# Performance work log

Hardware: AMD Instinct MI355X
Metric: run time of the kernel (lower is better)

Reference implementation:

```python
import jax, jax.numpy as jnp
import numpy as np

B = 32      # graphs per batch
N_NODES = 1024  # nodes per graph
K = 16      # top-k edges per node


def setup_inputs() -> dict:
    key = jax.random.key(0)
    k1, k2 = jax.random.split(key)
    x = jax.random.normal(k1, (B * N_NODES, 128), dtype=jnp.float32) * 0.1
    W = jax.random.normal(k2, (128, 64), dtype=jnp.float32) * (1.0 / np.sqrt(128))
    b = jnp.zeros((64,), dtype=jnp.float32)
    temperature = jnp.asarray(4.0, dtype=jnp.float32)
    return {"x": x, "W": W, "b": b, "temperature": temperature}


def reference(x, W, b, temperature):
    # Encoder: linear node embedding. out: [B*n, C]
    out = x @ W + b
    C = out.shape[-1]
    # Per-graph features, detached as in the original (graph_x = out[...].detach())
    h = jax.lax.stop_gradient(out).reshape(B, N_NODES, C)
    # Pairwise squared euclidean distances per graph: d[b,i,j] = ||h_i - h_j||^2
    sq = jnp.sum(h * h, axis=-1)  # [B, n]
    d_e = sq[:, :, None] + sq[:, None, :] - 2.0 * jnp.einsum('bic,bjc->bij', h, h)
    logits = jnp.exp(-temperature * d_e)  # [B, n, n]
    # Gumbel-noised top-k edge sampling
    z = jax.random.gumbel(jax.random.key(1), logits.shape, logits.dtype)
    _, edges_hat = jax.lax.top_k(logits + z, K)  # [B, n, K] int32
    # Build global edge index with cumulative per-graph node offsets
    offsets = (jnp.arange(B, dtype=jnp.int32) * N_NODES)[:, None, None]  # [B,1,1]
    rows = jnp.broadcast_to(jnp.arange(N_NODES, dtype=jnp.int32)[None, :, None] + offsets,
                            (B, N_NODES, K))
    cols = edges_hat.astype(jnp.int32) + offsets
    edges_idx = jnp.stack((rows.reshape(-1), cols.reshape(-1)))  # [2, B*n*K]
    return out, edges_idx
```

## Files before the change

### kernel.cpp

```cpp
#include <hip/hip_runtime.h>
#include <math.h>

#define OUT_ELEMS 2097152
#define EDGE_ELEMS 524288

__device__ __forceinline__ unsigned int rotl32(unsigned int x, int r){
  return (x << r) | (x >> (32 - r));
}

__device__ __forceinline__ unsigned int tf_bits_part(unsigned int e){
  unsigned int x0 = 0u, x1 = e;
  const unsigned int ks1 = 1u;
  const unsigned int ks2 = 0x1BD11BDBu;
  x1 += ks1;
#define TFR(r) { x0 += x1; x1 = rotl32(x1, r); x1 ^= x0; }
  TFR(13) TFR(15) TFR(26) TFR(6)
  x0 += ks1; x1 += ks2 + 1u;
  TFR(17) TFR(29) TFR(16) TFR(24)
  x0 += ks2; x1 += 0u + 2u;
  TFR(13) TFR(15) TFR(26) TFR(6)
  x0 += 0u;  x1 += ks1 + 3u;
  TFR(17) TFR(29) TFR(16) TFR(24)
  x0 += ks1; x1 += ks2 + 4u;
  TFR(13) TFR(15) TFR(26) TFR(6)
  x0 += ks2; x1 += 0u + 5u;
#undef TFR
  return x0 ^ x1;
}

__device__ __forceinline__ double rcp64(double x){
  double r;
  asm("v_rcp_f64 %0, %1" : "=v"(r) : "v"(x));
  double e = fma(-x, r, 1.0); r = fma(r, e, r);
  e = fma(-x, r, 1.0); r = fma(r, e, r);
  return r;
}

__device__ __forceinline__ double fast_exp(double x){
  double fn = __builtin_rint(x * 1.4426950408889634);
  int n = (int)fn;
  double r = fma(fn, -0.6931471803691238, x);
  r = fma(fn, -1.9082149292705877e-10, r);
  double p = 2.7557319223985893e-06;
  p = fma(r, p, 2.4801587301587302e-05);
  p = fma(r, p, 1.9841269841269841e-04);
  p = fma(r, p, 1.3888888888888889e-03);
  p = fma(r, p, 8.3333333333333333e-03);
  p = fma(r, p, 4.1666666666666664e-02);
  p = fma(r, p, 1.6666666666666666e-01);
  p = fma(r, p, 0.5);
  p = fma(r, p, 1.0);
  p = fma(r, p, 1.0);
  double scale = __longlong_as_double(((long long)(n + 1023)) << 52);
  return p * scale;
}

__device__ __forceinline__ double fast_log(double x){
  long long bx = __double_as_longlong(x);
  long long e = (bx >> 52) - 1023;
  double m = __longlong_as_double((bx & 0xFFFFFFFFFFFFFll) |
                                  0x3FF0000000000000ll);
  int big = m > 1.4142135623730951;
  m = big ? 0.5 * m : m;
  e += big;
  double s = (m - 1.0) * rcp64(m + 1.0);
  double s2 = s * s;
  double p = fma(s2, 2.0/11.0, 2.0/9.0);
  p = fma(s2, p, 2.0/7.0);
  p = fma(s2, p, 2.0/5.0);
  p = fma(s2, p, 2.0/3.0);
  double lm = fma(s * s2, p, 2.0 * s);
  return fma((double)e, 0.6931471805599453, lm);
}

__device__ __forceinline__ unsigned long long score_cand32(
    const float* __restrict__ og, const float* __restrict__ hrowf,
    unsigned int jc, unsigned int base, double Td, bool act){
  const float4* cp4 = (const float4*)(og + ((size_t)jc << 6));
  const float4* hp4 = (const float4*)hrowf;
  float a0 = 0.0f, a1 = 0.0f, a2 = 0.0f, a3 = 0.0f;
  #pragma unroll 4
  for (int ch = 0; ch < 16; ++ch){
    float4 cf = cp4[ch];
    float4 hf = hp4[ch];
    float d0 = hf.x - cf.x;
    float d1 = hf.y - cf.y;
    float d2 = hf.z - cf.z;
    float d3 = hf.w - cf.w;
    a0 = fmaf(d0, d0, a0);
    a1 = fmaf(d1, d1, a1);
    a2 = fmaf(d2, d2, a2);
    a3 = fmaf(d3, d3, a3);
  }
  if (!act) return 0ull;
  double acc = (double)((a0 + a1) + (a2 + a3));
  double sgm = fast_exp(-Td * acc);
  unsigned int bits = tf_bits_part(base | jc);
  float f = __uint_as_float(0x3f800000u | (bits >> 9)) - 1.0f;
  double u = (f > 0.0f) ? (double)f : 1.1754943508222875e-38;
  double w = -fast_log(u);
  double z = -fast_log(w);
  double sc = sgm + z;
  unsigned long long kb = (unsigned long long)__double_as_longlong(sc);
  kb ^= (unsigned long long)(((long long)kb) >> 63) | 0x8000000000000000ull;
  return (kb & ~1023ull) | (unsigned long long)(1023u - jc);
}

__device__ __forceinline__ unsigned long long bitonic64_desc(
    unsigned long long key, int lane){
  #pragma unroll
  for (int k = 2; k <= 64; k <<= 1){
    #pragma unroll
    for (int j = k >> 1; j; j >>= 1){
      unsigned long long o = __shfl_xor(key, j, 64);
      bool keep_hi = ((lane & k) == 0) == ((lane & j) == 0);
      key = (keep_hi == (o > key)) ? o : key;
    }
  }
  return key;
}

__device__ __forceinline__ unsigned int bitonic32_desc(
    unsigned int key, int lane){
  #pragma unroll
  for (int k = 2; k <= 64; k <<= 1){
    #pragma unroll
    for (int j = k >> 1; j; j >>= 1){
      unsigned int o = __shfl_xor(key, j, 64);
      bool keep_hi = ((lane & k) == 0) == ((lane & j) == 0);
      key = (keep_hi == (o > key)) ? o : key;
    }
  }
  return key;
}

__global__ __launch_bounds__(256) void cvt_wb_v16(
    const float* __restrict__ W, const float* __restrict__ b,
    double* __restrict__ w64, double* __restrict__ b64){
  const int i = blockIdx.x * 256 + threadIdx.x;
  if (i < 8192)      w64[i] = (double)W[i];
  else if (i < 8256) b64[i - 8192] = (double)b[i - 8192];
}

__global__ __launch_bounds__(512) void encoder_v16(
    const float* __restrict__ x, const double* __restrict__ w64,
    const double* __restrict__ b64, float* __restrict__ out){
  __shared__ float xs[64 * 129];
  const int tid = threadIdx.x;

  {
    const float4* xg4 = (const float4*)(x + ((size_t)blockIdx.x << 13));
    #pragma unroll
    for (int s = 0; s < 4; ++s){
      const int idx = tid + (s << 9);
      float4 v = xg4[idx];
      const int r = idx >> 5, k4 = (idx & 31) << 2;
      float* p = &xs[r * 129 + k4];
      p[0] = v.x; p[1] = v.y; p[2] = v.z; p[3] = v.w;
    }
  }
  __syncthreads();

  const int lane = tid & 63;
  const int wu = __builtin_amdgcn_readfirstlane(tid >> 6);
  const int c0 = wu << 3;
  const size_t row = ((size_t)blockIdx.x << 6) + (size_t)lane;

  double acc[8];
  const double* __restrict__ bp = b64 + c0;
  #pragma unroll
  for (int j = 0; j < 8; ++j) acc[j] = bp[j];

  const float* __restrict__ xrow = &xs[lane * 129];
  #pragma unroll 4
  for (int k = 0; k < 128; ++k){
    const double xk = (double)xrow[k];
    const double* __restrict__ wp = w64 + (k << 6) + c0;
    #pragma unroll
    for (int j = 0; j < 8; ++j)
      acc[j] = fma(xk, wp[j], acc[j]);
  }

  float* __restrict__ orow = out + (row << 6) + c0;
  #pragma unroll
  for (int j2 = 0; j2 < 4; ++j2){
    float2 st; st.x = (float)acc[(j2 << 1)]; st.y = (float)acc[(j2 << 1) + 1];
    *(float2*)&orow[j2 << 1] = st;
  }
}

__global__ __launch_bounds__(256, 8) void edges_v16(
    const float* __restrict__ out32, const float* __restrict__ temp,
    float* __restrict__ rows_out, float* __restrict__ cols_out){
  __shared__ float hidf[4][64];
  __shared__ unsigned int cl[4][128];
  const int tid = threadIdx.x, wave = tid >> 6, lane = tid & 63;
  const int gb = blockIdx.x >> 8;
  const int i0 = (blockIdx.x & 255) << 2;
  const int r  = i0 + wave;
  const float* __restrict__ og = out32 + ((size_t)gb << 16);

  hidf[wave][lane] = og[((size_t)r << 6) + lane];

  const unsigned int base = ((unsigned int)gb << 20) | ((unsigned int)r << 10);

  unsigned int v[16];
  unsigned int pmax = 0u;
  #pragma unroll
  for (int m = 0; m < 16; ++m){
    const unsigned int j = (unsigned int)(m << 6) + (unsigned int)lane;
    unsigned int bits = tf_bits_part(base | j);
    v[m] = (bits & ~1023u) | (1023u - j);
    pmax = (v[m] > pmax) ? v[m] : pmax;
  }

  unsigned int sorted = bitonic32_desc(pmax, lane);
  unsigned int b16p = __shfl(sorted, 15, 64);

  float u16 = __uint_as_float(0x3f800000u | (b16p >> 9)) - 1.0f;
  float z16 = -__logf(-__logf(u16));
  float uc  = __expf(-__expf(-(z16 - 1.001f)));
  unsigned int cp = ((__float_as_uint(1.0f + uc) & 0x7FFFFFu) << 9) & ~1023u;

  int cnt = 0;
  #pragma unroll
  for (int m = 0; m < 16; ++m) cnt += (v[m] >= cp) ? 1 : 0;
  int s = cnt;
  #pragma unroll
  for (int off = 1; off < 64; off <<= 1){
    int o = __shfl_up(s, off, 64);
    s += (lane >= off) ? o : 0;
  }
  int nc = __shfl(s, 63, 64);
  nc = (nc > 128) ? 128 : nc;
  int slot = s - cnt;
  #pragma unroll
  for (int m = 0; m < 16; ++m){
    if (v[m] >= cp && slot < 128){
      cl[wave][slot] = 1023u - (v[m] & 1023u);
      ++slot;
    }
  }

  const double Td = (double)temp[0];
  const bool act1 = (lane < nc);
  unsigned int jc1 = act1 ? cl[wave][lane] : 0u;
  unsigned long long key = score_cand32(og, &hidf[wave][0], jc1, base, Td, act1);
  key = bitonic64_desc(key, lane);

  if (nc > 64){
    const int idx2 = 64 + lane;
    const bool act2 = (idx2 < nc);
    unsigned int jc2 = act2 ? cl[wave][idx2] : 0u;
    unsigned long long k2 = score_cand32(og, &hidf[wave][0], jc2, base, Td, act2);
    k2 = bitonic64_desc(k2, lane);
    unsigned long long kr = __shfl(k2, 63 - lane, 64);
    key = (kr > key) ? kr : key;
    #pragma unroll
    for (int j = 32; j; j >>= 1){
      unsigned long long o = __shfl_xor(key, j, 64);
      bool left = (lane & j) == 0;
      bool take = left ? (o > key) : (o < key);
      key = take ? o : key;
    }
  }

  const int grow = (gb << 10) + r;
  if (lane < 16){
    rows_out[((size_t)grow << 4) + lane] = (float)grow;
    cols_out[((size_t)grow << 4) + lane] =
        (float)((gb << 10) + (1023 - (int)(key & 1023ull)));
  }
}

extern "C" void kernel_launch(void* const* d_in, const int* in_sizes, int n_in,
                              void* d_out, int out_size, void* d_ws, size_t ws_size,
                              hipStream_t stream){
  const float* x = (const float*)d_in[0];
  const float* W = (const float*)d_in[1];
  const float* b = (const float*)d_in[2];
  const float* T = (const float*)d_in[3];
  float* out      = (float*)d_out;
  float* rows_out = out + OUT_ELEMS;
  float* cols_out = rows_out + EDGE_ELEMS;

  double* w64 = (double*)d_ws;
  double* b64 = w64 + 8192;

  cvt_wb_v16<<<33, 256, 0, stream>>>(W, b, w64, b64);
  encoder_v16<<<512, 512, 0, stream>>>(x, w64, b64, out);
  edges_v16<<<8192, 256, 0, stream>>>(out, T, rows_out, cols_out);
}
```

Measured before the change: 178.1 us.

## Score candidates in fp32 with fp64 fallback on near-ties; cache Threefry bits

Candidate scoring (exp of negative scaled distance plus Gumbel noise) now runs in fp32 when there are at most 64 candidates. It falls back to the fp64 path only if adjacent top-16 scores are within a small margin. The Threefry random bits for each candidate are stored in shared memory next to its index, so they are not recomputed during scoring. This cuts the slow fp64 exp/log work on the common path, at the cost of a wider shared buffer, more live registers, and a correctness check that relies on the tie margin.

```diff
diff --git a/kernel.cpp b/kernel.cpp
--- a/kernel.cpp
+++ b/kernel.cpp
@@ -73,9 +73,9 @@
   return fma((double)e, 0.6931471805599453, lm);
 }
 
-__device__ __forceinline__ unsigned long long score_cand32(
+__device__ __forceinline__ float dist2_f32(
     const float* __restrict__ og, const float* __restrict__ hrowf,
-    unsigned int jc, unsigned int base, double Td, bool act){
+    unsigned int jc){
   const float4* cp4 = (const float4*)(og + ((size_t)jc << 6));
   const float4* hp4 = (const float4*)hrowf;
   float a0 = 0.0f, a1 = 0.0f, a2 = 0.0f, a3 = 0.0f;
@@ -92,18 +92,43 @@
     a2 = fmaf(d2, d2, a2);
     a3 = fmaf(d3, d3, a3);
   }
+  return (a0 + a1) + (a2 + a3);
+}
+
+__device__ __forceinline__ unsigned long long pack_key(double sc,
+                                                       unsigned int jc){
+  unsigned long long kb = (unsigned long long)__double_as_longlong(sc);
+  kb ^= (unsigned long long)(((long long)kb) >> 63) | 0x8000000000000000ull;
+  return (kb & ~1023ull) | (unsigned long long)(1023u - jc);
+}
+
+__device__ __forceinline__ unsigned long long tail64(
+    float accf, unsigned int bits, unsigned int jc, double Td, bool act){
   if (!act) return 0ull;
-  double acc = (double)((a0 + a1) + (a2 + a3));
-  double sgm = fast_exp(-Td * acc);
-  unsigned int bits = tf_bits_part(base | jc);
+  double sgm = fast_exp(-Td * (double)accf);
   float f = __uint_as_float(0x3f800000u | (bits >> 9)) - 1.0f;
   double u = (f > 0.0f) ? (double)f : 1.1754943508222875e-38;
   double w = -fast_log(u);
   double z = -fast_log(w);
   double sc = sgm + z;
-  unsigned long long kb = (unsigned long long)__double_as_longlong(sc);
-  kb ^= (unsigned long long)(((long long)kb) >> 63) | 0x8000000000000000ull;
-  return (kb & ~1023ull) | (unsigned long long)(1023u - jc);
+  return pack_key(sc, jc);
+}
+
+__device__ __forceinline__ unsigned long long tail32(
+    float accf, unsigned int bits, unsigned int jc, float Tf, bool act){
+  if (!act) return 0ull;
+  float sg = __expf(-Tf * accf);
+  float f = __uint_as_float(0x3f800000u | (bits >> 9)) - 1.0f;
+  float uf = (f > 0.0f) ? f : 1.17549435e-38f;
+  float wv = -__logf(uf);
+  float zf = -__logf(wv);
+  double sc = (double)sg + (double)zf;
+  return pack_key(sc, jc);
+}
+
+__device__ __forceinline__ double key_score(unsigned long long k){
+  unsigned long long orig = (k >> 63) ? (k ^ 0x8000000000000000ull) : ~k;
+  return __longlong_as_double((long long)(orig & ~1023ull));
 }
 
 __device__ __forceinline__ unsigned long long bitonic64_desc(
@@ -134,7 +159,7 @@
   return key;
 }
 
-__global__ __launch_bounds__(256) void cvt_wb_v16(
+__global__ __launch_bounds__(256) void cvt_wb_v17(
     const float* __restrict__ W, const float* __restrict__ b,
     double* __restrict__ w64, double* __restrict__ b64){
   const int i = blockIdx.x * 256 + threadIdx.x;
@@ -142,7 +167,7 @@
   else if (i < 8256) b64[i - 8192] = (double)b[i - 8192];
 }
 
-__global__ __launch_bounds__(512) void encoder_v16(
+__global__ __launch_bounds__(512) void encoder_v17(
     const float* __restrict__ x, const double* __restrict__ w64,
     const double* __restrict__ b64, float* __restrict__ out){
   __shared__ float xs[64 * 129];
@@ -189,11 +214,11 @@
   }
 }
 
-__global__ __launch_bounds__(256, 8) void edges_v16(
+__global__ __launch_bounds__(256, 8) void edges_v17(
     const float* __restrict__ out32, const float* __restrict__ temp,
     float* __restrict__ rows_out, float* __restrict__ cols_out){
   __shared__ float hidf[4][64];
-  __shared__ unsigned int cl[4][128];
+  __shared__ unsigned long long cl64[4][128];
   const int tid = threadIdx.x, wave = tid >> 6, lane = tid & 63;
   const int gb = blockIdx.x >> 8;
   const int i0 = (blockIdx.x & 255) << 2;
@@ -204,14 +229,14 @@
 
   const unsigned int base = ((unsigned int)gb << 20) | ((unsigned int)r << 10);
 
-  unsigned int v[16];
+  unsigned int b[16];
   unsigned int pmax = 0u;
   #pragma unroll
   for (int m = 0; m < 16; ++m){
     const unsigned int j = (unsigned int)(m << 6) + (unsigned int)lane;
-    unsigned int bits = tf_bits_part(base | j);
-    v[m] = (bits & ~1023u) | (1023u - j);
-    pmax = (v[m] > pmax) ? v[m] : pmax;
+    b[m] = tf_bits_part(base | j);
+    const unsigned int vm = (b[m] & ~1023u) | (1023u - j);
+    pmax = (vm > pmax) ? vm : pmax;
   }
 
   unsigned int sorted = bitonic32_desc(pmax, lane);
@@ -224,7 +249,11 @@
 
   int cnt = 0;
   #pragma unroll
-  for (int m = 0; m < 16; ++m) cnt += (v[m] >= cp) ? 1 : 0;
+  for (int m = 0; m < 16; ++m){
+    const unsigned int j = (unsigned int)(m << 6) + (unsigned int)lane;
+    const unsigned int vm = (b[m] & ~1023u) | (1023u - j);
+    cnt += (vm >= cp) ? 1 : 0;
+  }
   int s = cnt;
   #pragma unroll
   for (int off = 1; off < 64; off <<= 1){
@@ -236,30 +265,58 @@
   int slot = s - cnt;
   #pragma unroll
   for (int m = 0; m < 16; ++m){
-    if (v[m] >= cp && slot < 128){
-      cl[wave][slot] = 1023u - (v[m] & 1023u);
+    const unsigned int j = (unsigned int)(m << 6) + (unsigned int)lane;
+    const unsigned int vm = (b[m] & ~1023u) | (1023u - j);
+    if (vm >= cp && slot < 128){
+      cl64[wave][slot] = ((unsigned long long)b[m] << 32) |
+                         (unsigned long long)j;
       ++slot;
     }
   }
 
   const double Td = (double)temp[0];
-  const bool act1 = (lane < nc);
-  unsigned int jc1 = act1 ? cl[wave][lane] : 0u;
-  unsigned long long key = score_cand32(og, &hidf[wave][0], jc1, base, Td, act1);
-  key = bitonic64_desc(key, lane);
-
-  if (nc > 64){
+  const float  Tf = temp[0];
+  unsigned long long key;
+
+  if (nc <= 64){
+    const bool act1 = (lane < nc);
+    const unsigned long long e1 = act1 ? cl64[wave][lane] : 0ull;
+    const unsigned int jc1 = (unsigned int)(e1 & 1023ull);
+    const unsigned int bt1 = (unsigned int)(e1 >> 32);
+    const float ac1 = dist2_f32(og, &hidf[wave][0], jc1);
+    key = tail32(ac1, bt1, jc1, Tf, act1);
+    key = bitonic64_desc(key, lane);
+    double s0 = key_score(key);
+    unsigned long long kn = __shfl_down(key, 1, 64);
+    double s1 = key_score(kn);
+    bool tight = (lane < 16) && (key != 0ull) && ((s0 - s1) < 4e-5);
+    if (__any(tight)){
+      key = tail64(ac1, bt1, jc1, Td, act1);
+      key = bitonic64_desc(key, lane);
+    }
+  } else {
+    const bool act1 = (lane < nc);
+    const unsigned long long e1 = act1 ? cl64[wave][lane] : 0ull;
+    const unsigned int jc1 = (unsigned int)(e1 & 1023ull);
+    const unsigned int bt1 = (unsigned int)(e1 >> 32);
+    const float ac1 = dist2_f32(og, &hidf[wave][0], jc1);
+    key = tail64(ac1, bt1, jc1, Td, act1);
+    key = bitonic64_desc(key, lane);
+
     const int idx2 = 64 + lane;
     const bool act2 = (idx2 < nc);
-    unsigned int jc2 = act2 ? cl[wave][idx2] : 0u;
-    unsigned long long k2 = score_cand32(og, &hidf[wave][0], jc2, base, Td, act2);
+    const unsigned long long e2 = act2 ? cl64[wave][idx2] : 0ull;
+    const unsigned int jc2 = (unsigned int)(e2 & 1023ull);
+    const unsigned int bt2 = (unsigned int)(e2 >> 32);
+    const float ac2 = dist2_f32(og, &hidf[wave][0], jc2);
+    unsigned long long k2 = tail64(ac2, bt2, jc2, Td, act2);
     k2 = bitonic64_desc(k2, lane);
     unsigned long long kr = __shfl(k2, 63 - lane, 64);
     key = (kr > key) ? kr : key;
     #pragma unroll
-    for (int j = 32; j; j >>= 1){
-      unsigned long long o = __shfl_xor(key, j, 64);
-      bool left = (lane & j) == 0;
+    for (int j2 = 32; j2; j2 >>= 1){
+      unsigned long long o = __shfl_xor(key, j2, 64);
+      bool left = (lane & j2) == 0;
       bool take = left ? (o > key) : (o < key);
       key = take ? o : key;
     }
@@ -287,7 +344,7 @@
   double* w64 = (double*)d_ws;
   double* b64 = w64 + 8192;
 
-  cvt_wb_v16<<<33, 256, 0, stream>>>(W, b, w64, b64);
-  encoder_v16<<<512, 512, 0, stream>>>(x, w64, b64, out);
-  edges_v16<<<8192, 256, 0, stream>>>(out, T, rows_out, cols_out);
-}
+  cvt_wb_v17<<<33, 256, 0, stream>>>(W, b, w64, b64);
+  encoder_v17<<<512, 512, 0, stream>>>(x, w64, b64, out);
+  edges_v17<<<8192, 256, 0, stream>>>(out, T, rows_out, cols_out);
+}
```

Result: slower. 192.1 us (+7.8%).
